# Kernel tuning notes

Hardware: AMD Instinct MI355X
Metric: run time of the kernel (lower is better)

## Reference

```python
import jax, jax.numpy as jnp
import numpy as np

LX, LY = 256, 256
K_CLASSES = 4
N_SWEEPS = 2
N_SITES = LX * LY

# 8-neighborhood offsets (Moore neighborhood), border handled by clipping
_OFFSETS = np.array([[-1, -1], [-1, 0], [-1, 1],
                     [0, -1],           [0, 1],
                     [1, -1],  [1, 0],  [1, 1]], dtype=np.int32)


def setup_inputs() -> dict:
    key = jax.random.key(0)
    k1, k2, k3, k4 = jax.random.split(key, 4)
    X_init = jax.random.randint(k1, (LX, LY), 0, K_CLASSES).astype(jnp.int32)
    perm = jax.random.permutation(k2, jnp.arange(N_SITES)).astype(jnp.int32)
    uniforms = jax.random.uniform(k3, (N_SWEEPS, N_SITES), dtype=jnp.float32)
    beta = jax.random.uniform(k4, (), dtype=jnp.float32) + 0.5  # Potts coupling
    return {"X_init": X_init, "perm": perm, "uniforms": uniforms,
            "beta": beta, "K": K_CLASSES}


def reference(X_init, perm, uniforms, beta, K):
    lx, ly = X_init.shape
    off = jnp.asarray(_OFFSETS)              # (8, 2)
    classes = jnp.arange(K)                  # (K,)

    def update_one_site(X, uv, r):
        u, v = jnp.unravel_index(uv, (lx, ly))
        uu = jnp.clip(u + off[:, 0], 0, lx - 1)   # (8,) neighbor rows
        vv = jnp.clip(v + off[:, 1], 0, ly - 1)   # (8,) neighbor cols
        neigh = X[uu, vv]                          # (8,) dynamic gather
        # Potts potential: p_k proportional to exp(beta * #{neighbors == k})
        counts = (neigh[None, :] == classes[:, None]).sum(axis=1)  # (K,)
        probs = jax.nn.softmax(beta * counts.astype(jnp.float32))  # (K,) sums to 1
        # inverse-CDF categorical sample, as in the original cumsum < r
        x_sample = jnp.count_nonzero(jnp.cumsum(probs) < r)
        return X.at[u, v].set(x_sample.astype(X.dtype))  # scatter write

    def one_sweep(X, rs):
        def body(Xc, inp):
            uv, r = inp
            return update_one_site(Xc, uv, r), None
        X, _ = jax.lax.scan(body, X, (perm, rs))
        return X, None

    X_final, _ = jax.lax.scan(one_sweep, X_init, uniforms)  # N_SWEEPS sweeps
    return X_final
```

## Files before the change

kernel.cpp:

```cpp
#include <hip/hip_runtime.h>
#include <math.h>

#define NSITES 65536
#define WIN 8192
#define NW 8
#define KN 8
#define RMAX 64
#define MAGIC 0x51bb5eed


__device__ __forceinline__ int agg_pos(int v, int* c, int vmax) {
  int pos = 0;
  const int lane = threadIdx.x & 63;
  for (int vv = 1; vv <= vmax; ++vv) {
    unsigned long long m = __ballot(v == vv);
    if (m) {
      int leader = __ffsll((long long)m) - 1;
      int base = 0;
      if (lane == leader) base = atomicAdd(&c[vv], (int)__popcll(m));
      base = __shfl(base, leader);
      if (v == vv) pos = base + (int)__popcll(m & ((1ull << lane) - 1ull));
    }
  }
  return pos;
}

__device__ __forceinline__ void do_update(unsigned char* cell,
                                          const unsigned int* cellw,
                                          const float* c0a, const float* c1a,
                                          const float* c2a, const float* c3a,
                                          unsigned uvv, float r) {
  const int u = uvv >> 8, v = (int)(uvv & 255u);
  const int um = u ? u - 1 : 0, up = u < 255 ? u + 1 : 255;
  const int vm = v ? v - 1 : 0, vp = v < 255 ? v + 1 : 255;
  const int cb = vm >> 2;
  const int sh0 = (vm & 3) << 3;
  const int shv = (v - vm) << 3;
  const int shp = (vp - vm) << 3;
  int acc = 0;
  {
    const unsigned int* rw = cellw + (um << 6) + cb;
    const unsigned long long wd =
        ((unsigned long long)rw[1] << 32) | (unsigned long long)rw[0];
    const unsigned wl = (unsigned)(wd >> sh0);
    acc += 1 << ((wl & 255u) << 2);
    acc += 1 << (((wl >> shv) & 255u) << 2);
    acc += 1 << (((wl >> shp) & 255u) << 2);
  }
  {
    const unsigned int* rw = cellw + (u << 6) + cb;
    const unsigned long long wd =
        ((unsigned long long)rw[1] << 32) | (unsigned long long)rw[0];
    const unsigned wl = (unsigned)(wd >> sh0);
    acc += 1 << ((wl & 255u) << 2);
    acc += 1 << (((wl >> shp) & 255u) << 2);
  }
  {
    const unsigned int* rw = cellw + (up << 6) + cb;
    const unsigned long long wd =
        ((unsigned long long)rw[1] << 32) | (unsigned long long)rw[0];
    const unsigned wl = (unsigned)(wd >> sh0);
    acc += 1 << ((wl & 255u) << 2);
    acc += 1 << (((wl >> shv) & 255u) << 2);
    acc += 1 << (((wl >> shp) & 255u) << 2);
  }
  const int n0 = acc & 15, n1 = (acc >> 4) & 15, n2 = (acc >> 8) & 15;
  const int idx = n0 + 9 * n1 + 81 * n2;
  int cnt = (c0a[idx] < r) ? 1 : 0;
  cnt += (c1a[idx] < r) ? 1 : 0;
  cnt += (c2a[idx] < r) ? 1 : 0;
  cnt += (c3a[idx] < r) ? 1 : 0;
  cell[uvv] = (unsigned char)cnt;
}

__global__ __launch_bounds__(1024) void GibbsSampler_90443421319469_kernel(
    const int* __restrict__ Xi, const int* __restrict__ perm,
    const float* __restrict__ uni, const float* __restrict__ betap,
    uint2* __restrict__ recpk, int* __restrict__ ends, int* __restrict__ flags,
    int* __restrict__ out) {
#pragma clang fp contract(off)
  __shared__ __align__(16) unsigned char smem[147984];
  const int tid = threadIdx.x;

  if (blockIdx.x > 0) {
    const int w = blockIdx.x - 1;
    const int wbase = w * WIN;
    unsigned short* posg = (unsigned short*)smem;
    unsigned short* lvl = (unsigned short*)(smem + 131072);
    int* cnt = (int*)(smem + 147456);
    int* coff = cnt + 65;
    int* ctl = coff + 65;

    for (int g = tid; g < NSITES / 8; g += 1024)
      ((uint4*)posg)[g] = make_uint4(0u, 0u, 0u, 0u);
    if (tid <= RMAX) { cnt[tid] = 0; coff[tid] = 0; }
    if (tid == 0) { ctl[0] = 0; ctl[1] = 0; }
    __syncthreads();

    for (int k = 0; k < KN; ++k) {
      const int lt = k * 1024 + tid;
      posg[perm[wbase + lt]] = (unsigned short)(lt + 1);
    }
    __syncthreads();

    for (int c = 0; c < KN; ++c) {
      const int lt = c * 1024 + tid;
      const int uv = perm[wbase + lt];
      const int u = uv >> 8, v = uv & 255;
      const int um = u ? u - 1 : 0, up = u < 255 ? u + 1 : 255;
      const int vm = v ? v - 1 : 0, vp = v < 255 ? v + 1 : 255;
      const int nb8[8] = {(um << 8) | vm, (um << 8) | v, (um << 8) | vp,
                          (u << 8) | vm,                 (u << 8) | vp,
                          (up << 8) | vm, (up << 8) | v, (up << 8) | vp};
      int basemax = 0;
      unsigned long long q0 = 0ull, q1 = 0ull;
      int nin = 0;
#pragma unroll
      for (int j = 0; j < 8; ++j) {
        const int p = posg[nb8[j]];
        if (p && p - 1 < lt) {
          if (p - 1 < c * 1024) basemax = max(basemax, (int)lvl[p - 1]);
          else {
            q1 = (q1 << 16) | (q0 >> 48);
            q0 = (q0 << 16) | (unsigned long long)(p - 1);
            ++nin;
          }
        }
      }
      int ml = basemax + 1;
      lvl[lt] = (unsigned short)ml;
      __syncthreads();

      for (;;) {
        if (tid == 0) ctl[0] = 0;
        __syncthreads();
        bool ch = false;
        if (nin) {
          int m = basemax;
#pragma unroll
          for (int i = 0; i < 8; ++i) {
            if (i < nin) {
              const unsigned pp =
                  (unsigned)((i < 4 ? (q0 >> (16 * i)) : (q1 >> (16 * (i - 4))))
                             & 0xFFFFull);
              m = max(m, (int)lvl[pp]);
            }
          }
          const int nl = m + 1;
          if (nl != ml) { ml = nl; lvl[lt] = (unsigned short)nl; ch = true; }
        }
        if (ch) ctl[0] = 1;
        __syncthreads();
        if (ctl[0] == 0) break;
      }
    }

    {
      int mymax = 0;
#pragma unroll
      for (int k = 0; k < KN; ++k) mymax = max(mymax, (int)lvl[k * 1024 + tid]);
      atomicMax(&ctl[1], mymax);
    }
    __syncthreads();
    const int vmax = ctl[1];

#pragma unroll
    for (int k = 0; k < KN; ++k)
      (void)agg_pos((int)lvl[k * 1024 + tid], cnt, vmax);
    __syncthreads();
    if (tid == 0) {
      int e = 0;
      for (int r = 0; r < RMAX; ++r) {
        coff[r] = e;
        e += cnt[r];
        ends[w * RMAX + r] = e;
      }
    }
    __syncthreads();

    uint2* srec = (uint2*)posg;
#pragma unroll
    for (int k = 0; k < KN; ++k) {
      const int lt = k * 1024 + tid;
      const int pos = agg_pos((int)lvl[lt], coff, vmax);
      const unsigned uvv = (unsigned)perm[wbase + lt];
      srec[pos] = make_uint2(uvv, __float_as_uint(uni[wbase + lt]));
      srec[WIN + pos] =
          make_uint2(uvv, __float_as_uint(uni[NSITES + wbase + lt]));
    }
    __syncthreads();

    const uint4* s4 = (const uint4*)srec;
    uint4* d0 = (uint4*)(recpk + wbase);
    uint4* d1 = (uint4*)(recpk + NSITES + wbase);
    for (int g = tid; g < WIN / 2; g += 1024) {
      d0[g] = s4[g];
      d1[g] = s4[WIN / 2 + g];
    }
    __syncthreads();
    __threadfence();
    if (tid == 0) atomicExch(&flags[w], MAGIC);
    return;
  }

  unsigned int* cellw = (unsigned int*)smem;
  unsigned char* cell = (unsigned char*)smem;
  float* c0a = (float*)(smem + 65536);
  float* c1a = c0a + 729;
  float* c2a = c1a + 729;
  float* c3a = c2a + 729;
  int* lend = (int*)(smem + 65536 + 4 * 729 * 4);
  const float beta = betap[0];

  for (int g = tid; g < NSITES / 4; g += 1024) {
    int4 x = ((const int4*)Xi)[g];
    cellw[g] = (unsigned)(x.x & 255) | ((unsigned)(x.y & 255) << 8) |
               ((unsigned)(x.z & 255) << 16) | ((unsigned)(x.w & 255) << 24);
  }
  for (int t = tid; t < 729; t += 1024) {
    const int n0 = t % 9, n1 = (t / 9) % 9, n2 = t / 81;
    const int n3 = 8 - n0 - n1 - n2;
    float v0 = 2.f, v1 = 2.f, v2 = 2.f, v3 = 2.f;
    if (n3 >= 0) {
      const int mx = max(max(n0, n1), max(n2, n3));
      const float xm = beta * (float)mx;
      const float x0 = beta * (float)n0;
      const float x1 = beta * (float)n1;
      const float x2 = beta * (float)n2;
      const float x3 = beta * (float)n3;
      const float e0 = (float)exp((double)(x0 - xm));
      const float e1 = (float)exp((double)(x1 - xm));
      const float e2 = (float)exp((double)(x2 - xm));
      const float e3 = (float)exp((double)(x3 - xm));
      const float s = ((e0 + e1) + e2) + e3;
      v0 = e0 / s;
      v1 = v0 + e1 / s;
      v2 = v1 + e2 / s;
      v3 = v2 + e3 / s;
    }
    c0a[t] = v0; c1a[t] = v1; c2a[t] = v2; c3a[t] = v3;
  }
  __syncthreads();

  for (int w = 0; w < 2 * NW; ++w) {
    const int ww = w & (NW - 1);
    const int sw = w >> 3;

    if (w < NW) {
      if (tid == 0) {
        while (atomicAdd(&flags[ww], 0) != MAGIC) __builtin_amdgcn_s_sleep(8);
      }
      __syncthreads();
      __threadfence();
      if (tid < RMAX) lend[ww * RMAX + tid] = ends[ww * RMAX + tid];
      __syncthreads();
    }

    const uint2* rp = recpk + sw * NSITES + ww * WIN;
    const int* le = &lend[ww * RMAX];

    int nb = 0, ne = le[1];
    uint2 cur = make_uint2(0u, 0u);
    if (tid < ne) cur = rp[tid];

    for (int rd = 1; rd < RMAX; ++rd) {
      const int b = nb, e = ne;
      if (b >= WIN) break;

      if (WIN - b <= 64) {
        if (tid < 64) {
          const int i = b + tid;
          int myrd = 0;
          uint2 rc = make_uint2(0u, 0u);
          if (i < WIN) {
            myrd = rd;
            while (le[myrd] <= i) ++myrd;
            rc = rp[i];
          }
          int mx = myrd;
#pragma unroll
          for (int off = 1; off < 64; off <<= 1)
            mx = max(mx, __shfl_xor(mx, off));
          for (int rr = rd; rr <= mx; ++rr) {
            if (myrd == rr)
              do_update(cell, cellw, c0a, c1a, c2a, c3a, rc.x,
                        __uint_as_float(rc.y));
          }
        }
        __syncthreads();
        break;
      }

      nb = e;
      ne = (rd + 1 < RMAX) ? le[rd + 1] : e;
      uint2 nxt = make_uint2(0u, 0u);
      if (nb + tid < ne) nxt = rp[nb + tid];
      if (b + tid < e)
        do_update(cell, cellw, c0a, c1a, c2a, c3a, cur.x,
                  __uint_as_float(cur.y));
      for (int i = b + tid + 1024; i < e; i += 1024) {
        const uint2 rc = rp[i];
        do_update(cell, cellw, c0a, c1a, c2a, c3a, rc.x,
                  __uint_as_float(rc.y));
      }
      __syncthreads();
      cur = nxt;
    }
  }

  for (int g = tid; g < NSITES / 4; g += 1024) {
    const unsigned p = cellw[g];
    int4 o;
    o.x = (int)(p & 255u);
    o.y = (int)((p >> 8) & 255u);
    o.z = (int)((p >> 16) & 255u);
    o.w = (int)((p >> 24) & 255u);
    ((int4*)out)[g] = o;
  }
}

extern "C" void kernel_launch(void* const* d_in, const int* in_sizes, int n_in,
                              void* d_out, int out_size, void* d_ws,
                              size_t ws_size, hipStream_t stream) {
  const int* Xi = (const int*)d_in[0];
  const int* perm = (const int*)d_in[1];
  const float* uni = (const float*)d_in[2];
  const float* beta = (const float*)d_in[3];
  int* out = (int*)d_out;

  char* ws = (char*)d_ws;
  uint2* recpk = (uint2*)ws;
  int* ends = (int*)(ws + 2 * NSITES * 8);
  int* flags = (int*)(ws + 2 * NSITES * 8 + 2048);

  GibbsSampler_90443421319469_kernel<<<dim3(NW + 1), dim3(1024), 0, stream>>>(
      Xi, perm, uni, beta, recpk, ends, flags, out);
}
```

Baseline: 255.7 us.

## Merge per-chunk level relaxation loops into one global fixed-point iteration

The dependency-level computation in the preprocessing blocks used to run a separate relaxation loop for each of the 8 chunks, with two barriers per iteration. It now sets initial levels for all chunks, then runs one combined fixed-point loop over all chunks. Each pass uses a single barrier, and a per-pass change-flag array replaces the reset-then-check pattern on one shared flag. Perm values, neighbor lists and levels are kept in registers for reuse, which cuts shared and global reloads but raises register pressure at 1024 threads per block.

```diff
diff --git a/kernel.cpp b/kernel.cpp
--- a/kernel.cpp
+++ b/kernel.cpp
@@ -79,7 +79,7 @@
     uint2* __restrict__ recpk, int* __restrict__ ends, int* __restrict__ flags,
     int* __restrict__ out) {
 #pragma clang fp contract(off)
-  __shared__ __align__(16) unsigned char smem[147984];
+  __shared__ __align__(16) unsigned char smem[148240];
   const int tid = threadIdx.x;
 
   if (blockIdx.x > 0) {
@@ -90,83 +90,93 @@
     int* cnt = (int*)(smem + 147456);
     int* coff = cnt + 65;
     int* ctl = coff + 65;
+    int* chgar = ctl + 2;
 
     for (int g = tid; g < NSITES / 8; g += 1024)
       ((uint4*)posg)[g] = make_uint4(0u, 0u, 0u, 0u);
+    ((uint4*)lvl)[tid] = make_uint4(0u, 0u, 0u, 0u);
     if (tid <= RMAX) { cnt[tid] = 0; coff[tid] = 0; }
-    if (tid == 0) { ctl[0] = 0; ctl[1] = 0; }
-    __syncthreads();
-
+    if (tid < 64) chgar[tid] = 0;
+    if (tid == 0) ctl[0] = 0;
+    __syncthreads();
+
+    int uvk[KN];
+#pragma unroll
     for (int k = 0; k < KN; ++k) {
       const int lt = k * 1024 + tid;
-      posg[perm[wbase + lt]] = (unsigned short)(lt + 1);
-    }
-    __syncthreads();
-
+      uvk[k] = perm[wbase + lt];
+      posg[uvk[k]] = (unsigned short)(lt + 1);
+    }
+    __syncthreads();
+
+    unsigned long long q0[KN], q1[KN];
+    int nin[KN], ml[KN];
+#pragma unroll
     for (int c = 0; c < KN; ++c) {
       const int lt = c * 1024 + tid;
-      const int uv = perm[wbase + lt];
-      const int u = uv >> 8, v = uv & 255;
+      const int uv = uvk[c], u = uv >> 8, v = uv & 255;
       const int um = u ? u - 1 : 0, up = u < 255 ? u + 1 : 255;
       const int vm = v ? v - 1 : 0, vp = v < 255 ? v + 1 : 255;
       const int nb8[8] = {(um << 8) | vm, (um << 8) | v, (um << 8) | vp,
                           (u << 8) | vm,                 (u << 8) | vp,
                           (up << 8) | vm, (up << 8) | v, (up << 8) | vp};
-      int basemax = 0;
-      unsigned long long q0 = 0ull, q1 = 0ull;
-      int nin = 0;
+      unsigned long long a0 = 0ull, a1 = 0ull;
+      int nn = 0, bm = 0;
 #pragma unroll
       for (int j = 0; j < 8; ++j) {
         const int p = posg[nb8[j]];
         if (p && p - 1 < lt) {
-          if (p - 1 < c * 1024) basemax = max(basemax, (int)lvl[p - 1]);
-          else {
-            q1 = (q1 << 16) | (q0 >> 48);
-            q0 = (q0 << 16) | (unsigned long long)(p - 1);
-            ++nin;
-          }
+          a1 = (a1 << 16) | (a0 >> 48);
+          a0 = (a0 << 16) | (unsigned long long)(p - 1);
+          ++nn;
+          bm = max(bm, (int)lvl[p - 1]);
         }
       }
-      int ml = basemax + 1;
-      lvl[lt] = (unsigned short)ml;
-      __syncthreads();
-
-      for (;;) {
-        if (tid == 0) ctl[0] = 0;
-        __syncthreads();
-        bool ch = false;
-        if (nin) {
-          int m = basemax;
+      q0[c] = a0; q1[c] = a1; nin[c] = nn;
+      ml[c] = bm + 1;
+      lvl[lt] = (unsigned short)ml[c];
+      __syncthreads();
+    }
+
+    for (int pass = 0; pass < 63; ++pass) {
+      bool ch = false;
+#pragma unroll
+      for (int c = 0; c < KN; ++c) {
+        if (nin[c]) {
+          int m = 0;
 #pragma unroll
           for (int i = 0; i < 8; ++i) {
-            if (i < nin) {
+            if (i < nin[c]) {
               const unsigned pp =
-                  (unsigned)((i < 4 ? (q0 >> (16 * i)) : (q1 >> (16 * (i - 4))))
-                             & 0xFFFFull);
+                  (unsigned)((i < 4 ? (q0[c] >> (16 * i))
+                                    : (q1[c] >> (16 * (i - 4)))) & 0xFFFFull);
               m = max(m, (int)lvl[pp]);
             }
           }
           const int nl = m + 1;
-          if (nl != ml) { ml = nl; lvl[lt] = (unsigned short)nl; ch = true; }
+          if (nl != ml[c]) {
+            ml[c] = nl;
+            lvl[c * 1024 + tid] = (unsigned short)nl;
+            ch = true;
+          }
         }
-        if (ch) ctl[0] = 1;
-        __syncthreads();
-        if (ctl[0] == 0) break;
-      }
+      }
+      if (ch) chgar[pass] = 1;
+      __syncthreads();
+      if (chgar[pass] == 0) break;
     }
 
     {
-      int mymax = 0;
-#pragma unroll
-      for (int k = 0; k < KN; ++k) mymax = max(mymax, (int)lvl[k * 1024 + tid]);
-      atomicMax(&ctl[1], mymax);
-    }
-    __syncthreads();
-    const int vmax = ctl[1];
-
-#pragma unroll
-    for (int k = 0; k < KN; ++k)
-      (void)agg_pos((int)lvl[k * 1024 + tid], cnt, vmax);
+      int mym = 0;
+#pragma unroll
+      for (int k = 0; k < KN; ++k) mym = max(mym, ml[k]);
+      atomicMax(&ctl[0], mym);
+    }
+    __syncthreads();
+    const int vmax = ctl[0];
+
+#pragma unroll
+    for (int k = 0; k < KN; ++k) (void)agg_pos(ml[k], cnt, vmax);
     __syncthreads();
     if (tid == 0) {
       int e = 0;
@@ -182,8 +192,8 @@
 #pragma unroll
     for (int k = 0; k < KN; ++k) {
       const int lt = k * 1024 + tid;
-      const int pos = agg_pos((int)lvl[lt], coff, vmax);
-      const unsigned uvv = (unsigned)perm[wbase + lt];
+      const int pos = agg_pos(ml[k], coff, vmax);
+      const unsigned uvv = (unsigned)uvk[k];
       srec[pos] = make_uint2(uvv, __float_as_uint(uni[wbase + lt]));
       srec[WIN + pos] =
           make_uint2(uvv, __float_as_uint(uni[NSITES + wbase + lt]));
```

Result: no change. 254.7 us (-0.4%).
